# Kernel tuning notes

Hardware: AMD Instinct MI355X
Metric: run time of the kernel (lower is better)

Reference implementation:

```python
import jax, jax.numpy as jnp
import numpy as np

WIN_SIZE = 9  # (2*win_rad+1)^2 with win_rad=1
EPS = 1e-7   # compute_laplacian default eps


def _windows(a):
    """Sliding 3x3 window extraction: (H, W, ...) -> (H-2, W-2, 9, ...)."""
    H, W = a.shape[0], a.shape[1]
    ch, cw = H - 2, W - 2
    return jnp.stack([a[dy:dy + ch, dx:dx + cw] for dy in range(3) for dx in range(3)], axis=2)


def _laplacian_vals(img):
    """Per-window matting Laplacian blocks. img: (H, W, 3) -> vals: (N, 9, 9)."""
    winI = _windows(img).reshape(-1, WIN_SIZE, 3)                      # (N, 9, 3)
    mu = winI.mean(axis=1, keepdims=True)                              # (N, 1, 3)
    var = (jnp.einsum('nji,njk->nik', winI, winI) / WIN_SIZE
           - jnp.einsum('nji,njk->nik', mu, mu))                       # (N, 3, 3)
    inv = jnp.linalg.inv(var + (EPS / WIN_SIZE) * jnp.eye(3, dtype=img.dtype))
    Xc = winI - mu                                                     # (N, 9, 3)
    X = jnp.einsum('nij,njk->nik', Xc, inv)                            # (N, 9, 3)
    vals = jnp.eye(WIN_SIZE, dtype=img.dtype) - (1.0 + jnp.einsum('nij,nkj->nik', X, Xc)) / WIN_SIZE
    return vals                                                        # (N, 9, 9)


def _win_inds(H, W):
    """Flat pixel indices of each 3x3 window: (N, 9) int32. Static given H, W."""
    idx = jnp.arange(H * W, dtype=jnp.int32).reshape(H, W)
    return _windows(idx).reshape(-1, WIN_SIZE)


def setup_inputs() -> dict:
    key = jax.random.key(0)
    k1, k2 = jax.random.split(key)
    B, C, H, W = 4, 3, 512, 512
    output = jax.random.normal(k1, (B, C, H, W), dtype=jnp.float32)
    content = jax.random.uniform(k2, (B, C, H, W), dtype=jnp.float32)
    return {"output": output, "content": content}


def reference(output, content):
    B, C, H, W = output.shape
    img = jnp.moveaxis(content, 1, 3)          # (B, H, W, 3)
    inds = _win_inds(H, W)                     # (N, 9) constant index map

    def per_image(im, out):
        vals = _laplacian_vals(im)             # (N, 9, 9)
        xw = out.reshape(C, H * W)[:, inds]    # (C, N, 9) gather per window
        # sum over channels/windows of x_win^T L_win x_win == sum_c x_c^T L x_c
        return jnp.einsum('nij,cni,cnj->', vals, xw, xw)

    loss = jax.vmap(per_image)(img, output)    # (B,)
    return loss.reshape(B, 1, 1)
```

## Files before the change

### kernel.cpp

```cpp
#include <hip/hip_runtime.h>

#define EPSV 1e-7f

typedef float f2 __attribute__((ext_vector_type(2)));

__global__ __launch_bounds__(256) void matting_loss_kernel(
    const float* __restrict__ outp, const float* __restrict__ cont,
    float* __restrict__ ws)
{
    const int H = 512, W = 512, NW = 510;
    const int HW = H * W;

    const int lin = blockIdx.x + 8 * (blockIdx.y + 64 * blockIdx.z);
    const int swz = (lin & 7) * 256 + (lin >> 3);
    const int b   = swz >> 9;
    const int rem = swz & 511;
    const int gx  = (rem & 7) * 32 + threadIdx.x;
    const int gy  = (rem >> 3) * 8 + threadIdx.y;
    const int wx0 = gx * 2;
    const int wy  = gy;

    const float* Cin = cont + (size_t)b * 3 * HW;
    const float* Xin = outp + (size_t)b * 3 * HW;

    float contrib = 0.0f;
    const float inv9 = 1.0f / 9.0f;

#define WSUM(OUT, A0, A1) { f2 T_ = (A0) + (A1); (OUT).x = T_.x + (A0).y; (OUT).y = T_.y + (A1).x; }
#define CSUM(CH, OUT) { \
    f2 A0_ = Cb[CH][0][0] + Cb[CH][1][0] + Cb[CH][2][0]; \
    f2 A1_ = Cb[CH][0][1] + Cb[CH][1][1] + Cb[CH][2][1]; \
    WSUM(OUT, A0_, A1_) }
#define CDOT(CA, CB_, OUT) { \
    f2 A0_ = Cb[CA][0][0]*Cb[CB_][0][0] + Cb[CA][1][0]*Cb[CB_][1][0] + Cb[CA][2][0]*Cb[CB_][2][0]; \
    f2 A1_ = Cb[CA][0][1]*Cb[CB_][0][1] + Cb[CA][1][1]*Cb[CB_][1][1] + Cb[CA][2][1]*Cb[CB_][2][1]; \
    WSUM(OUT, A0_, A1_) }
#define XSUM(C_, OUT) { \
    f2 A0_ = Xb[C_][0][0] + Xb[C_][1][0] + Xb[C_][2][0]; \
    f2 A1_ = Xb[C_][0][1] + Xb[C_][1][1] + Xb[C_][2][1]; \
    WSUM(OUT, A0_, A1_) }
#define XXDOT(C_, OUT) { \
    f2 A0_ = Xb[C_][0][0]*Xb[C_][0][0] + Xb[C_][1][0]*Xb[C_][1][0] + Xb[C_][2][0]*Xb[C_][2][0]; \
    f2 A1_ = Xb[C_][0][1]*Xb[C_][0][1] + Xb[C_][1][1]*Xb[C_][1][1] + Xb[C_][2][1]*Xb[C_][2][1]; \
    WSUM(OUT, A0_, A1_) }
#define XCDOT(C_, K_, OUT) { \
    f2 A0_ = Xb[C_][0][0]*Cb[K_][0][0] + Xb[C_][1][0]*Cb[K_][1][0] + Xb[C_][2][0]*Cb[K_][2][0]; \
    f2 A1_ = Xb[C_][0][1]*Cb[K_][0][1] + Xb[C_][1][1]*Cb[K_][1][1] + Xb[C_][2][1]*Cb[K_][2][1]; \
    WSUM(OUT, A0_, A1_) }

    if (wy < NW && wx0 < NW) {
        const int base = wy * W + wx0;

        f2 Cb[3][3][2];
        f2 Xb[3][3][2];
        #pragma unroll
        for (int ch = 0; ch < 3; ++ch)
            #pragma unroll
            for (int r = 0; r < 3; ++r) {
                const float* p = Cin + ch * HW + base + r * W;
                Cb[ch][r][0] = *(const f2*)p;
                Cb[ch][r][1] = *(const f2*)(p + 2);
                const float* q = Xin + ch * HW + base + r * W;
                Xb[ch][r][0] = *(const f2*)q;
                Xb[ch][r][1] = *(const f2*)(q + 2);
            }

        f2 sI0, sI1, sI2, s00, s01, s02, s11, s12, s22;
        CSUM(0, sI0) CSUM(1, sI1) CSUM(2, sI2)
        CDOT(0, 0, s00) CDOT(0, 1, s01) CDOT(0, 2, s02)
        CDOT(1, 1, s11) CDOT(1, 2, s12) CDOT(2, 2, s22)

        f2 mu0 = sI0 * inv9, mu1 = sI1 * inv9, mu2 = sI2 * inv9;
        const float ed = EPSV * inv9;
        f2 v00 = s00 * inv9 - mu0 * mu0 + ed;
        f2 v01 = s01 * inv9 - mu0 * mu1;
        f2 v02 = s02 * inv9 - mu0 * mu2;
        f2 v11 = s11 * inv9 - mu1 * mu1 + ed;
        f2 v12 = s12 * inv9 - mu1 * mu2;
        f2 v22 = s22 * inv9 - mu2 * mu2 + ed;
        f2 adj0 = v11 * v22 - v12 * v12;
        f2 adj1 = v02 * v12 - v01 * v22;
        f2 adj2 = v01 * v12 - v02 * v11;
        f2 adj3 = v00 * v22 - v02 * v02;
        f2 adj4 = v01 * v02 - v00 * v12;
        f2 adj5 = v00 * v11 - v01 * v01;
        f2 det = v00 * adj0 + v01 * adj1 + v02 * adj2;
        f2 id;
        id.x = __builtin_amdgcn_rcpf(det.x);
        id.y = __builtin_amdgcn_rcpf(det.y);

        f2 termAcc = (f2){0.0f, 0.0f};
        #pragma unroll
        for (int c = 0; c < 3; ++c) {
            f2 S, SSw, W0, W1, W2;
            XSUM(c, S) XXDOT(c, SSw)
            XCDOT(c, 0, W0) XCDOT(c, 1, W1) XCDOT(c, 2, W2)
            f2 u0 = W0 - S * mu0;
            f2 u1 = W1 - S * mu1;
            f2 u2 = W2 - S * mu2;
            f2 qa = u0 * (adj0 * u0 + adj1 * u1 + adj2 * u2)
                  + u1 * (adj1 * u0 + adj3 * u1 + adj4 * u2)
                  + u2 * (adj2 * u0 + adj4 * u1 + adj5 * u2);
            termAcc += SSw - (S * S + qa * id) * inv9;
        }
        contrib = termAcc.x + termAcc.y;
    }
#undef WSUM
#undef CSUM
#undef CDOT
#undef XSUM
#undef XXDOT
#undef XCDOT

    #pragma unroll
    for (int off = 32; off > 0; off >>= 1)
        contrib += __shfl_down(contrib, off, 64);

    __shared__ float wsum[4];
    const int tid = threadIdx.y * 32 + threadIdx.x;
    const int lane = tid & 63, wv = tid >> 6;
    if (lane == 0) wsum[wv] = contrib;
    __syncthreads();
    if (tid == 0)
        ws[swz] = wsum[0] + wsum[1] + wsum[2] + wsum[3];
}

__global__ __launch_bounds__(256) void reduce_kernel(
    const float* __restrict__ ws, float* __restrict__ loss)
{
    const int b = blockIdx.x;
    const int t = threadIdx.x;
    float v = ws[b * 512 + t] + ws[b * 512 + 256 + t];
    #pragma unroll
    for (int off = 32; off > 0; off >>= 1)
        v += __shfl_down(v, off, 64);

    __shared__ float s[4];
    if ((t & 63) == 0) s[t >> 6] = v;
    __syncthreads();
    if (t == 0) loss[b] = s[0] + s[1] + s[2] + s[3];
}

extern "C" void kernel_launch(void* const* d_in, const int* in_sizes, int n_in,
                              void* d_out, int out_size, void* d_ws, size_t ws_size,
                              hipStream_t stream) {
    const float* outp = (const float*)d_in[0];
    const float* cont = (const float*)d_in[1];
    float* loss = (float*)d_out;
    float* ws   = (float*)d_ws;

    dim3 block(32, 8, 1);
    dim3 grid(8, 64, 4);
    matting_loss_kernel<<<grid, block, 0, stream>>>(outp, cont, ws);
    reduce_kernel<<<dim3(4, 1, 1), dim3(256, 1, 1), 0, stream>>>(ws, loss);
}
```

Baseline: 14.90 us.

## Compute 2x2 windows per thread to share overlapping row loads

```diff
diff --git a/kernel.cpp b/kernel.cpp
--- a/kernel.cpp
+++ b/kernel.cpp
@@ -11,14 +11,14 @@
     const int H = 512, W = 512, NW = 510;
     const int HW = H * W;
 
-    const int lin = blockIdx.x + 8 * (blockIdx.y + 64 * blockIdx.z);
-    const int swz = (lin & 7) * 256 + (lin >> 3);
-    const int b   = swz >> 9;
-    const int rem = swz & 511;
+    const int lin = blockIdx.x + 8 * (blockIdx.y + 32 * blockIdx.z);
+    const int swz = (lin & 7) * 128 + (lin >> 3);
+    const int b   = swz >> 8;
+    const int rem = swz & 255;
     const int gx  = (rem & 7) * 32 + threadIdx.x;
-    const int gy  = (rem >> 3) * 8 + threadIdx.y;
+    const int gg  = (rem >> 3) * 8 + threadIdx.y;
     const int wx0 = gx * 2;
-    const int wy  = gy;
+    const int wy0 = gg * 2;
 
     const float* Cin = cont + (size_t)b * 3 * HW;
     const float* Xin = outp + (size_t)b * 3 * HW;
@@ -27,81 +27,94 @@
     const float inv9 = 1.0f / 9.0f;
 
 #define WSUM(OUT, A0, A1) { f2 T_ = (A0) + (A1); (OUT).x = T_.x + (A0).y; (OUT).y = T_.y + (A1).x; }
-#define CSUM(CH, OUT) { \
-    f2 A0_ = Cb[CH][0][0] + Cb[CH][1][0] + Cb[CH][2][0]; \
-    f2 A1_ = Cb[CH][0][1] + Cb[CH][1][1] + Cb[CH][2][1]; \
+#define CSUM(CH, R0, OUT) { \
+    f2 A0_ = Cb[CH][R0][0] + Cb[CH][R0+1][0] + Cb[CH][R0+2][0]; \
+    f2 A1_ = Cb[CH][R0][1] + Cb[CH][R0+1][1] + Cb[CH][R0+2][1]; \
     WSUM(OUT, A0_, A1_) }
-#define CDOT(CA, CB_, OUT) { \
-    f2 A0_ = Cb[CA][0][0]*Cb[CB_][0][0] + Cb[CA][1][0]*Cb[CB_][1][0] + Cb[CA][2][0]*Cb[CB_][2][0]; \
-    f2 A1_ = Cb[CA][0][1]*Cb[CB_][0][1] + Cb[CA][1][1]*Cb[CB_][1][1] + Cb[CA][2][1]*Cb[CB_][2][1]; \
+#define CDOT(CA, CB_, R0, OUT) { \
+    f2 A0_ = Cb[CA][R0][0]*Cb[CB_][R0][0] + Cb[CA][R0+1][0]*Cb[CB_][R0+1][0] + Cb[CA][R0+2][0]*Cb[CB_][R0+2][0]; \
+    f2 A1_ = Cb[CA][R0][1]*Cb[CB_][R0][1] + Cb[CA][R0+1][1]*Cb[CB_][R0+1][1] + Cb[CA][R0+2][1]*Cb[CB_][R0+2][1]; \
     WSUM(OUT, A0_, A1_) }
-#define XSUM(C_, OUT) { \
-    f2 A0_ = Xb[C_][0][0] + Xb[C_][1][0] + Xb[C_][2][0]; \
-    f2 A1_ = Xb[C_][0][1] + Xb[C_][1][1] + Xb[C_][2][1]; \
+#define XSUM(R0, OUT) { \
+    f2 A0_ = Xb[R0][0] + Xb[R0+1][0] + Xb[R0+2][0]; \
+    f2 A1_ = Xb[R0][1] + Xb[R0+1][1] + Xb[R0+2][1]; \
     WSUM(OUT, A0_, A1_) }
-#define XXDOT(C_, OUT) { \
-    f2 A0_ = Xb[C_][0][0]*Xb[C_][0][0] + Xb[C_][1][0]*Xb[C_][1][0] + Xb[C_][2][0]*Xb[C_][2][0]; \
-    f2 A1_ = Xb[C_][0][1]*Xb[C_][0][1] + Xb[C_][1][1]*Xb[C_][1][1] + Xb[C_][2][1]*Xb[C_][2][1]; \
+#define XXDOT(R0, OUT) { \
+    f2 A0_ = Xb[R0][0]*Xb[R0][0] + Xb[R0+1][0]*Xb[R0+1][0] + Xb[R0+2][0]*Xb[R0+2][0]; \
+    f2 A1_ = Xb[R0][1]*Xb[R0][1] + Xb[R0+1][1]*Xb[R0+1][1] + Xb[R0+2][1]*Xb[R0+2][1]; \
     WSUM(OUT, A0_, A1_) }
-#define XCDOT(C_, K_, OUT) { \
-    f2 A0_ = Xb[C_][0][0]*Cb[K_][0][0] + Xb[C_][1][0]*Cb[K_][1][0] + Xb[C_][2][0]*Cb[K_][2][0]; \
-    f2 A1_ = Xb[C_][0][1]*Cb[K_][0][1] + Xb[C_][1][1]*Cb[K_][1][1] + Xb[C_][2][1]*Cb[K_][2][1]; \
+#define XCDOT(R0, K_, OUT) { \
+    f2 A0_ = Xb[R0][0]*Cb[K_][R0][0] + Xb[R0+1][0]*Cb[K_][R0+1][0] + Xb[R0+2][0]*Cb[K_][R0+2][0]; \
+    f2 A1_ = Xb[R0][1]*Cb[K_][R0][1] + Xb[R0+1][1]*Cb[K_][R0+1][1] + Xb[R0+2][1]*Cb[K_][R0+2][1]; \
     WSUM(OUT, A0_, A1_) }
 
-    if (wy < NW && wx0 < NW) {
-        const int base = wy * W + wx0;
+    if (wy0 < NW && wx0 < NW) {
+        const int base = wy0 * W + wx0;
 
-        f2 Cb[3][3][2];
-        f2 Xb[3][3][2];
+        f2 Cb[3][4][2];
         #pragma unroll
         for (int ch = 0; ch < 3; ++ch)
             #pragma unroll
-            for (int r = 0; r < 3; ++r) {
+            for (int r = 0; r < 4; ++r) {
                 const float* p = Cin + ch * HW + base + r * W;
                 Cb[ch][r][0] = *(const f2*)p;
                 Cb[ch][r][1] = *(const f2*)(p + 2);
-                const float* q = Xin + ch * HW + base + r * W;
-                Xb[ch][r][0] = *(const f2*)q;
-                Xb[ch][r][1] = *(const f2*)(q + 2);
             }
 
-        f2 sI0, sI1, sI2, s00, s01, s02, s11, s12, s22;
-        CSUM(0, sI0) CSUM(1, sI1) CSUM(2, sI2)
-        CDOT(0, 0, s00) CDOT(0, 1, s01) CDOT(0, 2, s02)
-        CDOT(1, 1, s11) CDOT(1, 2, s12) CDOT(2, 2, s22)
-
-        f2 mu0 = sI0 * inv9, mu1 = sI1 * inv9, mu2 = sI2 * inv9;
-        const float ed = EPSV * inv9;
-        f2 v00 = s00 * inv9 - mu0 * mu0 + ed;
-        f2 v01 = s01 * inv9 - mu0 * mu1;
-        f2 v02 = s02 * inv9 - mu0 * mu2;
-        f2 v11 = s11 * inv9 - mu1 * mu1 + ed;
-        f2 v12 = s12 * inv9 - mu1 * mu2;
-        f2 v22 = s22 * inv9 - mu2 * mu2 + ed;
-        f2 adj0 = v11 * v22 - v12 * v12;
-        f2 adj1 = v02 * v12 - v01 * v22;
-        f2 adj2 = v01 * v12 - v02 * v11;
-        f2 adj3 = v00 * v22 - v02 * v02;
-        f2 adj4 = v01 * v02 - v00 * v12;
-        f2 adj5 = v00 * v11 - v01 * v01;
-        f2 det = v00 * adj0 + v01 * adj1 + v02 * adj2;
-        f2 id;
-        id.x = __builtin_amdgcn_rcpf(det.x);
-        id.y = __builtin_amdgcn_rcpf(det.y);
+        f2 mu0[2], mu1[2], mu2[2];
+        f2 adj0[2], adj1[2], adj2[2], adj3[2], adj4[2], adj5[2], idet[2];
+        #pragma unroll
+        for (int wr = 0; wr < 2; ++wr) {
+            f2 sI0, sI1, sI2, s00, s01, s02, s11, s12, s22;
+            CSUM(0, wr, sI0) CSUM(1, wr, sI1) CSUM(2, wr, sI2)
+            CDOT(0, 0, wr, s00) CDOT(0, 1, wr, s01) CDOT(0, 2, wr, s02)
+            CDOT(1, 1, wr, s11) CDOT(1, 2, wr, s12) CDOT(2, 2, wr, s22)
+            f2 m0 = sI0 * inv9, m1 = sI1 * inv9, m2 = sI2 * inv9;
+            const float ed = EPSV * inv9;
+            f2 v00 = s00 * inv9 - m0 * m0 + ed;
+            f2 v01 = s01 * inv9 - m0 * m1;
+            f2 v02 = s02 * inv9 - m0 * m2;
+            f2 v11 = s11 * inv9 - m1 * m1 + ed;
+            f2 v12 = s12 * inv9 - m1 * m2;
+            f2 v22 = s22 * inv9 - m2 * m2 + ed;
+            f2 a0 = v11 * v22 - v12 * v12;
+            f2 a1 = v02 * v12 - v01 * v22;
+            f2 a2 = v01 * v12 - v02 * v11;
+            f2 det = v00 * a0 + v01 * a1 + v02 * a2;
+            mu0[wr] = m0; mu1[wr] = m1; mu2[wr] = m2;
+            adj0[wr] = a0; adj1[wr] = a1; adj2[wr] = a2;
+            adj3[wr] = v00 * v22 - v02 * v02;
+            adj4[wr] = v01 * v02 - v00 * v12;
+            adj5[wr] = v00 * v11 - v01 * v01;
+            f2 idv;
+            idv.x = __builtin_amdgcn_rcpf(det.x);
+            idv.y = __builtin_amdgcn_rcpf(det.y);
+            idet[wr] = idv;
+        }
 
         f2 termAcc = (f2){0.0f, 0.0f};
         #pragma unroll
         for (int c = 0; c < 3; ++c) {
-            f2 S, SSw, W0, W1, W2;
-            XSUM(c, S) XXDOT(c, SSw)
-            XCDOT(c, 0, W0) XCDOT(c, 1, W1) XCDOT(c, 2, W2)
-            f2 u0 = W0 - S * mu0;
-            f2 u1 = W1 - S * mu1;
-            f2 u2 = W2 - S * mu2;
-            f2 qa = u0 * (adj0 * u0 + adj1 * u1 + adj2 * u2)
-                  + u1 * (adj1 * u0 + adj3 * u1 + adj4 * u2)
-                  + u2 * (adj2 * u0 + adj4 * u1 + adj5 * u2);
-            termAcc += SSw - (S * S + qa * id) * inv9;
+            f2 Xb[4][2];
+            #pragma unroll
+            for (int r = 0; r < 4; ++r) {
+                const float* q = Xin + c * HW + base + r * W;
+                Xb[r][0] = *(const f2*)q;
+                Xb[r][1] = *(const f2*)(q + 2);
+            }
+            #pragma unroll
+            for (int wr = 0; wr < 2; ++wr) {
+                f2 S, SSw, W0, W1, W2;
+                XSUM(wr, S) XXDOT(wr, SSw)
+                XCDOT(wr, 0, W0) XCDOT(wr, 1, W1) XCDOT(wr, 2, W2)
+                f2 u0 = W0 - S * mu0[wr];
+                f2 u1 = W1 - S * mu1[wr];
+                f2 u2 = W2 - S * mu2[wr];
+                f2 qa = u0 * (adj0[wr] * u0 + adj1[wr] * u1 + adj2[wr] * u2)
+                      + u1 * (adj1[wr] * u0 + adj3[wr] * u1 + adj4[wr] * u2)
+                      + u2 * (adj2[wr] * u0 + adj4[wr] * u1 + adj5[wr] * u2);
+                termAcc += SSw - (S * S + qa * idet[wr]) * inv9;
+            }
         }
         contrib = termAcc.x + termAcc.y;
     }
@@ -130,7 +143,7 @@
 {
     const int b = blockIdx.x;
     const int t = threadIdx.x;
-    float v = ws[b * 512 + t] + ws[b * 512 + 256 + t];
+    float v = ws[b * 256 + t];
     #pragma unroll
     for (int off = 32; off > 0; off >>= 1)
         v += __shfl_down(v, off, 64);
@@ -150,7 +163,7 @@
     float* ws   = (float*)d_ws;
 
     dim3 block(32, 8, 1);
-    dim3 grid(8, 64, 4);
+    dim3 grid(8, 32, 4);
     matting_loss_kernel<<<grid, block, 0, stream>>>(outp, cont, ws);
     reduce_kernel<<<dim3(4, 1, 1), dim3(256, 1, 1), 0, stream>>>(ws, loss);
 }
```

New measurement: 13.78 us, median of 3. 7.6% less time.
